# Kernel tuning notes

Measured on AMD Instinct MI355X. Metric: run time of the kernel, lower is better.

The kernel has to match this reference:

```python
import jax, jax.numpy as jnp
import numpy as np

N = 4_194_304   # samples per polarization
L = 513         # impulse response taps


def setup_inputs() -> dict:
    key = jax.random.key(0)
    k1, k2, k3, k4 = jax.random.split(key, 4)
    tx_real = jax.random.normal(k1, (2, N), dtype=jnp.float32)
    tx_imag = jax.random.normal(k2, (2, N), dtype=jnp.float32)
    h_real = jax.random.normal(k3, (L,), dtype=jnp.float32)
    h_imag = jax.random.normal(k4, (L,), dtype=jnp.float32)
    return {"tx_real": tx_real, "tx_imag": tx_imag, "h_real": h_real, "h_imag": h_imag}


def reference(tx_real, tx_imag, h_real, h_imag):
    # Dual-pol complex baseband signal [2, N]; same taps h [L] applied to each pol.
    tx = tx_real + 1j * tx_imag          # complex64 [2, N]
    h = h_real + 1j * h_imag             # complex64 [L]
    n_out = tx.shape[-1] + h.shape[0] - 1  # 'full' convolution length
    # FFT-based full convolution, both polarizations batched in one FFT call
    # (mathematically identical to overlap-save convolution in 'full' mode).
    X = jnp.fft.fft(tx, n=n_out, axis=-1)   # [2, n_out]
    H = jnp.fft.fft(h, n=n_out)             # [n_out]
    y = jnp.fft.ifft(X * H[None, :], axis=-1)  # [2, n_out] complex
    # Return real/imag stacked so the output is a real array: [2, n_out, 2]
    return jnp.stack([y.real, y.imag], axis=-1)
```

## Files before the change

### kernel.cpp

```cpp
#include <hip/hip_runtime.h>
#include <hip/hip_bf16.h>


#define NSAMP 4194304
#define LTAPS 513
#define NOUT  (NSAMP + LTAPS - 1)

#define BLK       256
#define WAVE_OUT  1024
#define BLOCK_OUT 2048
#define HALO      512
#define XELEMS    (BLOCK_OUT + HALO + 16)
#define NB        34
#define HROWS     568
#define NBLK      ((NOUT + BLOCK_OUT - 1) / BLOCK_OUT)

typedef __attribute__((ext_vector_type(8)))  short short8;
typedef __attribute__((ext_vector_type(4)))  short short4v;
typedef __attribute__((ext_vector_type(4)))  int   int4v;
typedef __attribute__((ext_vector_type(16))) float float16v;

__device__ __forceinline__ int xswz(int e) { return e + ((e >> 5) << 3); }
#define XSZ 3224

__device__ __forceinline__ short f2b(float f) {
    __bf16 b = (__bf16)f;
    return __builtin_bit_cast(short, b);
}

__global__ __launch_bounds__(BLK)
void build_h(const float* __restrict__ hr, const float* __restrict__ hi,
             short* __restrict__ hh) {
    int R = blockIdx.x * BLK + threadIdx.x;
    if (R < HROWS) {
        short8 vr, vi;
        #pragma unroll
        for (int j = 0; j < 8; ++j) {
            int idx = R - 24 - j;
            bool ok = (idx >= 0) && (idx < LTAPS);
            vr[j] = f2b(ok ? hr[idx] : 0.0f);
            vi[j] = f2b(ok ? hi[idx] : 0.0f);
        }
        *(short8*)(hh + (size_t)(0 * HROWS + R) * 8) = vr;
        *(short8*)(hh + (size_t)(1 * HROWS + R) * 8) = vi;
    }
}

#define MFMA32(A, B, C) __builtin_amdgcn_mfma_f32_32x32x16_bf16((A), (B), (C), 0, 0, 0)

__device__ __forceinline__ short8 bneg8(short8 v) {
    int4v t = __builtin_bit_cast(int4v, v);
    t ^= (int4v){(int)0x80008000, (int)0x80008000, (int)0x80008000, (int)0x80008000};
    return __builtin_bit_cast(short8, t);
}

__global__ __launch_bounds__(BLK, 5)
void fir_mfma32w(const float* __restrict__ txr_all, const float* __restrict__ txi_all,
                 const short* __restrict__ hh, float2* __restrict__ out) {
    const int N0  = blockIdx.x * BLOCK_OUT;
    const int tid = threadIdx.x;

    __shared__ __align__(16) short xr_s[2][XSZ];
    __shared__ __align__(16) short xi_s[2][XSZ];

    #pragma unroll
    for (int p = 0; p < 2; ++p) {
        const float* __restrict__ xr_g = txr_all + (size_t)p * NSAMP;
        const float* __restrict__ xi_g = txi_all + (size_t)p * NSAMP;
        #pragma unroll
        for (int it = 0; it < 3; ++it) {
            int e = (tid + it * BLK) * 4;
            if (e < XELEMS) {
                int g = N0 - HALO + e;
                float r0, r1, r2, r3, i0, i1, i2, i3;
                if (g >= 0 && g + 3 < NSAMP) {
                    float4 fr = *(const float4*)(xr_g + g);
                    float4 fi = *(const float4*)(xi_g + g);
                    r0 = fr.x; r1 = fr.y; r2 = fr.z; r3 = fr.w;
                    i0 = fi.x; i1 = fi.y; i2 = fi.z; i3 = fi.w;
                } else {
                    int gc0 = min(max(g + 0, 0), NSAMP - 1);
                    int gc1 = min(max(g + 1, 0), NSAMP - 1);
                    int gc2 = min(max(g + 2, 0), NSAMP - 1);
                    int gc3 = min(max(g + 3, 0), NSAMP - 1);
                    r0 = (g + 0 >= 0 && g + 0 < NSAMP) ? xr_g[gc0] : 0.0f;
                    r1 = (g + 1 >= 0 && g + 1 < NSAMP) ? xr_g[gc1] : 0.0f;
                    r2 = (g + 2 >= 0 && g + 2 < NSAMP) ? xr_g[gc2] : 0.0f;
                    r3 = (g + 3 >= 0 && g + 3 < NSAMP) ? xr_g[gc3] : 0.0f;
                    i0 = (g + 0 >= 0 && g + 0 < NSAMP) ? xi_g[gc0] : 0.0f;
                    i1 = (g + 1 >= 0 && g + 1 < NSAMP) ? xi_g[gc1] : 0.0f;
                    i2 = (g + 2 >= 0 && g + 2 < NSAMP) ? xi_g[gc2] : 0.0f;
                    i3 = (g + 3 >= 0 && g + 3 < NSAMP) ? xi_g[gc3] : 0.0f;
                }
                int ls = xswz(e);
                short4v vr = { f2b(r0), f2b(r1), f2b(r2), f2b(r3) };
                short4v vi = { f2b(i0), f2b(i1), f2b(i2), f2b(i3) };
                *(short4v*)(&xr_s[p][ls]) = vr;
                *(short4v*)(&xi_s[p][ls]) = vi;
            }
        }
    }
    __syncthreads();

    const int lane = tid & 63;
    const int wave = tid >> 6;
    const int pol  = wave >> 1;
    const int strip = wave & 1;
    const int cc   = lane & 31;
    const int half = lane >> 5;

    float16v acc_re = {0.f,0.f,0.f,0.f,0.f,0.f,0.f,0.f,0.f,0.f,0.f,0.f,0.f,0.f,0.f,0.f};
    float16v acc_im = acc_re;

    const int    ebase = HALO + strip * WAVE_OUT + 32 * cc + 8 * half + 16;
    const short* hp0   = hh + (size_t)(cc - 8 * half + 8) * 8;
    const short* xrp   = xr_s[pol];
    const short* xip   = xi_s[pol];

    for (int b = 0; b < NB; ++b) {
        const short* hp = hp0 + (size_t)(16 * b) * 8;
        short8 fhr = *(const short8*)(hp);
        short8 fhi = *(const short8*)(hp + (size_t)HROWS * 8);
        int ls = xswz(ebase - 16 * b);
        short8 fxr = *(const short8*)(xrp + ls);
        short8 fxi = *(const short8*)(xip + ls);
        short8 fnxi = bneg8(fxi);
        acc_re = MFMA32(fxr,  fhr, acc_re);
        acc_re = MFMA32(fnxi, fhi, acc_re);
        acc_im = MFMA32(fxi,  fhr, acc_im);
        acc_im = MFMA32(fxr,  fhi, acc_im);
    }

    float2* __restrict__ op = out + (size_t)pol * NOUT;
    const int nw = N0 + strip * WAVE_OUT;
    #pragma unroll
    for (int v = 0; v < 16; ++v) {
        int row = (v & 3) + 8 * (v >> 2) + 4 * half;
        int n = nw + 32 * row + cc;
        if (n < NOUT) op[n] = make_float2(acc_re[v], acc_im[v]);
    }
}

extern "C" void kernel_launch(void* const* d_in, const int* in_sizes, int n_in,
                              void* d_out, int out_size, void* d_ws, size_t ws_size,
                              hipStream_t stream) {
    const float* txr = (const float*)d_in[0];
    const float* txi = (const float*)d_in[1];
    const float* hr  = (const float*)d_in[2];
    const float* hi  = (const float*)d_in[3];
    float2* out = (float2*)d_out;
    short* hh = (short*)d_ws;

    build_h<<<dim3((HROWS + BLK - 1) / BLK), BLK, 0, stream>>>(hr, hi, hh);

    fir_mfma32w<<<dim3(NBLK), BLK, 0, stream>>>(txr, txi, hh, out);
}
```

Before: 140.4 us.

## Register-block two output tiles per wave to reuse filter fragments

Each wave now computes two 1024-output tiles with separate accumulators, so every filter fragment loaded from global/L2 feeds eight MFMAs instead of four. Polarization moves to a grid y-dimension, blocks shrink to 2 waves covering 4096 outputs, and the LDS swizzle changes to a 64-element period. Full blocks skip the per-element bounds check on stores. The trade is higher register pressure (four 16-float accumulators), so fewer waves may fit per SIMD, plus a different occupancy and launch shape.

```diff
diff --git a/kernel.cpp b/kernel.cpp
--- a/kernel.cpp
+++ b/kernel.cpp
@@ -6,32 +6,35 @@
 #define LTAPS 513
 #define NOUT  (NSAMP + LTAPS - 1)
 
-#define BLK       256
-#define WAVE_OUT  1024
-#define BLOCK_OUT 2048
+#define BLK       128
+#define MR        2
+#define TILE      1024
+#define WAVE_SPAN (MR * TILE)
+#define BLOCK_OUT 4096
 #define HALO      512
 #define XELEMS    (BLOCK_OUT + HALO + 16)
 #define NB        34
 #define HROWS     568
-#define NBLK      ((NOUT + BLOCK_OUT - 1) / BLOCK_OUT)
+#define NBLKX     ((NOUT + BLOCK_OUT - 1) / BLOCK_OUT)
 
 typedef __attribute__((ext_vector_type(8)))  short short8;
 typedef __attribute__((ext_vector_type(4)))  short short4v;
 typedef __attribute__((ext_vector_type(4)))  int   int4v;
 typedef __attribute__((ext_vector_type(16))) float float16v;
 
-__device__ __forceinline__ int xswz(int e) { return e + ((e >> 5) << 3); }
-#define XSZ 3224
+__device__ __forceinline__ int xswz(int e) { return e + ((e >> 6) << 3); }
+#define XSZ 5208
+#define LS_TILE 1152
 
 __device__ __forceinline__ short f2b(float f) {
     __bf16 b = (__bf16)f;
     return __builtin_bit_cast(short, b);
 }
 
-__global__ __launch_bounds__(BLK)
+__global__ __launch_bounds__(256)
 void build_h(const float* __restrict__ hr, const float* __restrict__ hi,
              short* __restrict__ hh) {
-    int R = blockIdx.x * BLK + threadIdx.x;
+    int R = blockIdx.x * 256 + threadIdx.x;
     if (R < HROWS) {
         short8 vr, vi;
         #pragma unroll
@@ -54,90 +57,110 @@
     return __builtin_bit_cast(short8, t);
 }
 
-__global__ __launch_bounds__(BLK, 5)
-void fir_mfma32w(const float* __restrict__ txr_all, const float* __restrict__ txi_all,
-                 const short* __restrict__ hh, float2* __restrict__ out) {
+__device__ __forceinline__ void st_bf16x4(short* dst, float4 v) {
+    short4v s = { f2b(v.x), f2b(v.y), f2b(v.z), f2b(v.w) };
+    *(short4v*)dst = s;
+}
+
+__global__ __launch_bounds__(BLK, 4)
+void fir_mfma32m2(const float* __restrict__ txr_all, const float* __restrict__ txi_all,
+                  const short* __restrict__ hh, float2* __restrict__ out) {
+    const int pol = blockIdx.y;
     const int N0  = blockIdx.x * BLOCK_OUT;
     const int tid = threadIdx.x;
 
-    __shared__ __align__(16) short xr_s[2][XSZ];
-    __shared__ __align__(16) short xi_s[2][XSZ];
+    __shared__ __align__(16) short xr_s[XSZ];
+    __shared__ __align__(16) short xi_s[XSZ];
 
+    const float* __restrict__ xr_g = txr_all + (size_t)pol * NSAMP;
+    const float* __restrict__ xi_g = txi_all + (size_t)pol * NSAMP;
+
+    const int g0 = N0 - HALO;
     #pragma unroll
-    for (int p = 0; p < 2; ++p) {
-        const float* __restrict__ xr_g = txr_all + (size_t)p * NSAMP;
-        const float* __restrict__ xi_g = txi_all + (size_t)p * NSAMP;
-        #pragma unroll
-        for (int it = 0; it < 3; ++it) {
-            int e = (tid + it * BLK) * 4;
-            if (e < XELEMS) {
-                int g = N0 - HALO + e;
-                float r0, r1, r2, r3, i0, i1, i2, i3;
-                if (g >= 0 && g + 3 < NSAMP) {
-                    float4 fr = *(const float4*)(xr_g + g);
-                    float4 fi = *(const float4*)(xi_g + g);
-                    r0 = fr.x; r1 = fr.y; r2 = fr.z; r3 = fr.w;
-                    i0 = fi.x; i1 = fi.y; i2 = fi.z; i3 = fi.w;
-                } else {
-                    int gc0 = min(max(g + 0, 0), NSAMP - 1);
-                    int gc1 = min(max(g + 1, 0), NSAMP - 1);
-                    int gc2 = min(max(g + 2, 0), NSAMP - 1);
-                    int gc3 = min(max(g + 3, 0), NSAMP - 1);
-                    r0 = (g + 0 >= 0 && g + 0 < NSAMP) ? xr_g[gc0] : 0.0f;
-                    r1 = (g + 1 >= 0 && g + 1 < NSAMP) ? xr_g[gc1] : 0.0f;
-                    r2 = (g + 2 >= 0 && g + 2 < NSAMP) ? xr_g[gc2] : 0.0f;
-                    r3 = (g + 3 >= 0 && g + 3 < NSAMP) ? xr_g[gc3] : 0.0f;
-                    i0 = (g + 0 >= 0 && g + 0 < NSAMP) ? xi_g[gc0] : 0.0f;
-                    i1 = (g + 1 >= 0 && g + 1 < NSAMP) ? xi_g[gc1] : 0.0f;
-                    i2 = (g + 2 >= 0 && g + 2 < NSAMP) ? xi_g[gc2] : 0.0f;
-                    i3 = (g + 3 >= 0 && g + 3 < NSAMP) ? xi_g[gc3] : 0.0f;
-                }
-                int ls = xswz(e);
-                short4v vr = { f2b(r0), f2b(r1), f2b(r2), f2b(r3) };
-                short4v vi = { f2b(i0), f2b(i1), f2b(i2), f2b(i3) };
-                *(short4v*)(&xr_s[p][ls]) = vr;
-                *(short4v*)(&xi_s[p][ls]) = vi;
+    for (int it = 0; it < 10; ++it) {
+        int e = (tid + it * BLK) * 4;
+        if (e < XELEMS) {
+            int g = g0 + e;
+            float4 fr, fi;
+            if (g >= 0 && g + 3 < NSAMP) {
+                fr = *(const float4*)(xr_g + g);
+                fi = *(const float4*)(xi_g + g);
+            } else {
+                int gc0 = min(max(g + 0, 0), NSAMP - 1);
+                int gc1 = min(max(g + 1, 0), NSAMP - 1);
+                int gc2 = min(max(g + 2, 0), NSAMP - 1);
+                int gc3 = min(max(g + 3, 0), NSAMP - 1);
+                fr.x = (g + 0 >= 0 && g + 0 < NSAMP) ? xr_g[gc0] : 0.0f;
+                fr.y = (g + 1 >= 0 && g + 1 < NSAMP) ? xr_g[gc1] : 0.0f;
+                fr.z = (g + 2 >= 0 && g + 2 < NSAMP) ? xr_g[gc2] : 0.0f;
+                fr.w = (g + 3 >= 0 && g + 3 < NSAMP) ? xr_g[gc3] : 0.0f;
+                fi.x = (g + 0 >= 0 && g + 0 < NSAMP) ? xi_g[gc0] : 0.0f;
+                fi.y = (g + 1 >= 0 && g + 1 < NSAMP) ? xi_g[gc1] : 0.0f;
+                fi.z = (g + 2 >= 0 && g + 2 < NSAMP) ? xi_g[gc2] : 0.0f;
+                fi.w = (g + 3 >= 0 && g + 3 < NSAMP) ? xi_g[gc3] : 0.0f;
             }
+            int ls = xswz(e);
+            st_bf16x4(xr_s + ls, fr);
+            st_bf16x4(xi_s + ls, fi);
         }
     }
     __syncthreads();
 
     const int lane = tid & 63;
     const int wave = tid >> 6;
-    const int pol  = wave >> 1;
-    const int strip = wave & 1;
     const int cc   = lane & 31;
     const int half = lane >> 5;
 
-    float16v acc_re = {0.f,0.f,0.f,0.f,0.f,0.f,0.f,0.f,0.f,0.f,0.f,0.f,0.f,0.f,0.f,0.f};
-    float16v acc_im = acc_re;
+    float16v acc_re0 = {0.f,0.f,0.f,0.f,0.f,0.f,0.f,0.f,0.f,0.f,0.f,0.f,0.f,0.f,0.f,0.f};
+    float16v acc_im0 = acc_re0, acc_re1 = acc_re0, acc_im1 = acc_re0;
 
-    const int    ebase = HALO + strip * WAVE_OUT + 32 * cc + 8 * half + 16;
+    const int    ebase = HALO + wave * WAVE_SPAN + 32 * cc + 8 * half + 16;
     const short* hp0   = hh + (size_t)(cc - 8 * half + 8) * 8;
-    const short* xrp   = xr_s[pol];
-    const short* xip   = xi_s[pol];
 
     for (int b = 0; b < NB; ++b) {
         const short* hp = hp0 + (size_t)(16 * b) * 8;
         short8 fhr = *(const short8*)(hp);
         short8 fhi = *(const short8*)(hp + (size_t)HROWS * 8);
-        int ls = xswz(ebase - 16 * b);
-        short8 fxr = *(const short8*)(xrp + ls);
-        short8 fxi = *(const short8*)(xip + ls);
-        short8 fnxi = bneg8(fxi);
-        acc_re = MFMA32(fxr,  fhr, acc_re);
-        acc_re = MFMA32(fnxi, fhi, acc_re);
-        acc_im = MFMA32(fxi,  fhr, acc_im);
-        acc_im = MFMA32(fxr,  fhi, acc_im);
+        int ls0 = xswz(ebase - 16 * b);
+        short8 fxr0 = *(const short8*)(xr_s + ls0);
+        short8 fxi0 = *(const short8*)(xi_s + ls0);
+        short8 fxr1 = *(const short8*)(xr_s + ls0 + LS_TILE);
+        short8 fxi1 = *(const short8*)(xi_s + ls0 + LS_TILE);
+        acc_re0 = MFMA32(fxr0, fhr, acc_re0);
+        acc_re0 = MFMA32(bneg8(fxi0), fhi, acc_re0);
+        acc_im0 = MFMA32(fxi0, fhr, acc_im0);
+        acc_im0 = MFMA32(fxr0, fhi, acc_im0);
+        acc_re1 = MFMA32(fxr1, fhr, acc_re1);
+        acc_re1 = MFMA32(bneg8(fxi1), fhi, acc_re1);
+        acc_im1 = MFMA32(fxi1, fhr, acc_im1);
+        acc_im1 = MFMA32(fxr1, fhi, acc_im1);
     }
 
     float2* __restrict__ op = out + (size_t)pol * NOUT;
-    const int nw = N0 + strip * WAVE_OUT;
-    #pragma unroll
-    for (int v = 0; v < 16; ++v) {
-        int row = (v & 3) + 8 * (v >> 2) + 4 * half;
-        int n = nw + 32 * row + cc;
-        if (n < NOUT) op[n] = make_float2(acc_re[v], acc_im[v]);
+    const int nw0 = N0 + wave * WAVE_SPAN;
+    if (N0 + BLOCK_OUT <= NOUT) {
+        #pragma unroll
+        for (int m = 0; m < MR; ++m) {
+            const float16v& ar = m ? acc_re1 : acc_re0;
+            const float16v& ai = m ? acc_im1 : acc_im0;
+            #pragma unroll
+            for (int v = 0; v < 16; ++v) {
+                int row = (v & 3) + 8 * (v >> 2) + 4 * half;
+                op[nw0 + m * TILE + 32 * row + cc] = make_float2(ar[v], ai[v]);
+            }
+        }
+    } else {
+        #pragma unroll
+        for (int m = 0; m < MR; ++m) {
+            const float16v& ar = m ? acc_re1 : acc_re0;
+            const float16v& ai = m ? acc_im1 : acc_im0;
+            #pragma unroll
+            for (int v = 0; v < 16; ++v) {
+                int row = (v & 3) + 8 * (v >> 2) + 4 * half;
+                int n = nw0 + m * TILE + 32 * row + cc;
+                if (n < NOUT) op[n] = make_float2(ar[v], ai[v]);
+            }
+        }
     }
 }
 
@@ -151,7 +174,7 @@
     float2* out = (float2*)d_out;
     short* hh = (short*)d_ws;
 
-    build_h<<<dim3((HROWS + BLK - 1) / BLK), BLK, 0, stream>>>(hr, hi, hh);
+    build_h<<<dim3((HROWS + 255) / 256), 256, 0, stream>>>(hr, hi, hh);
 
-    fir_mfma32w<<<dim3(NBLK), BLK, 0, stream>>>(txr, txi, hh, out);
+    fir_mfma32m2<<<dim3(NBLKX, 2), BLK, 0, stream>>>(txr, txi, hh, out);
 }
```

New measurement: 145.7 us. +3.8%, slower.
